# Kernel tuning notes

Measured on AMD Instinct MI355X. Metric: run time of the kernel, lower is better.

## Reference

```python
import jax, jax.numpy as jnp
import numpy as np

SR = 16000
BLOCK_SIZE = 160
N_WT = 64
WT_LEN = 512
SEC = 60
T = SR * SEC  # 960000 samples
FRAMES = 100 * SEC  # 6000 attention frames


def _make_sine_table(length, cycle, phase):
    i = np.arange(length, dtype=np.float32)
    wt = np.sin(cycle * 2 * np.pi * i / length + 2 * phase * np.pi).astype(np.float32)
    wt[-1] = wt[0]  # loop-closing trick: last sample = first sample
    return wt


def setup_inputs() -> dict:
    key = jax.random.key(0)
    k1, k2, k3, k4 = jax.random.split(key, 4)
    pitch = jax.random.uniform(k1, (1, T, 1), dtype=jnp.float32) * 360.0 + 40.0  # 40..400 Hz
    amplitude = jax.random.uniform(k2, (1, T, 1), dtype=jnp.float32)
    # wavetables: first 4 are fixed sine harmonics with wrapped endpoint, rest learned
    rng = np.random.default_rng(0)
    wts = np.asarray(jax.random.normal(k3, (N_WT, WT_LEN), dtype=jnp.float32)) * 0.01
    for idx in range(4):
        wts[idx] = _make_sine_table(WT_LEN, idx + 1, rng.uniform(0.0, 1.0))
    wts[4:, -1] = wts[4:, 0]  # wrap endpoint for learned tables too
    attention = jax.random.normal(k4, (N_WT, FRAMES), dtype=jnp.float32)
    return {
        "pitch": pitch,
        "amplitude": amplitude,
        "wavetables": jnp.asarray(wts),
        "attention": attention,
        "sec": SEC,
    }


def reference(pitch, amplitude, wavetables, attention, sec):
    L = wavetables.shape[1]
    freq = pitch.reshape(-1)  # [T], torch .squeeze()
    inc = freq / SR * L  # phase increment per sample
    # exclusive cumulative sum: cumsum(inc) - inc  (matches cumsum - increment[0] broadcast)
    idx = (jnp.cumsum(inc) - inc) % L  # [T]
    lo = jnp.floor(idx)
    hi = jnp.ceil(idx)
    alpha = idx - lo  # fractional part
    lo_i = lo.astype(jnp.int32)
    hi_i = hi.astype(jnp.int32) % L
    # tanh applied to learned tables (idx >= 4); fixed sine tables passed through
    wts_eff = jnp.concatenate([wavetables[:4], jnp.tanh(wavetables[4:])], axis=0)  # [64, L]
    w_lo = wts_eff[:, lo_i]  # [64, T] gather
    w_hi = wts_eff[:, hi_i]  # [64, T] gather
    osc = w_lo + alpha[None, :] * (w_hi - w_lo)  # [64, T] linear interp
    att = jax.nn.softmax(attention, axis=0)  # softmax over wavetables
    att_up = jnp.repeat(att, BLOCK_SIZE, axis=1)  # nearest-neighbor upsample -> [64, T]
    mixed = jnp.sum(osc * att_up, axis=0)  # [T]
    return mixed[None, :, None] * amplitude  # [1, T, 1]
```

## Files before the change

kernel.cpp:

```cpp
#include <hip/hip_runtime.h>
#include <math.h>

#define BLKSZ 160
#define NWT   64
#define WTLEN 512
#define FPB   8
#define SPB   1280
#define NTHR  256
#define SMP   12

#define NB1   3750
#define NB2   235
#define NB2P  240
#define NB3   15

#define PRI(a)  ((a) + ((a) >> 4))

static __device__ __forceinline__ float inc32_of(float p) {
    return (p / 16000.0f) * 512.0f;
}

__global__ __launch_bounds__(256) void k_leaf(
    const float* __restrict__ pitch, const float* __restrict__ wts,
    float* __restrict__ bs1, float* __restrict__ bs2,
    float* __restrict__ wts_eff, int T)
{
    int t = threadIdx.x;
    if (blockIdx.x >= NB2) {
        int i = (blockIdx.x - NB2) * 256 + t;
        if (i < NWT * WTLEN) {
            float v = wts[i];
            if ((i >> 9) >= 4) v = tanhf(v);
            wts_eff[i] = v;
        }
        return;
    }
    __shared__ float b0[256];
    __shared__ float b1[16];
    int blk = blockIdx.x;
    size_t s0 = (size_t)blk * 4096;
    int nsamp = min(4096, T - (int)s0);
    int nb0 = nsamp >> 4;
    if (t < nb0) {
        const float4* p4 = (const float4*)(pitch + s0 + (size_t)t * 16);
        float acc = 0.f;
        #pragma unroll
        for (int i = 0; i < 4; ++i) {
            float4 v = p4[i];
            acc = acc + inc32_of(v.x);
            acc = acc + inc32_of(v.y);
            acc = acc + inc32_of(v.z);
            acc = acc + inc32_of(v.w);
        }
        b0[t] = acc;
    }
    __syncthreads();
    int nb1 = nb0 >> 4;
    if (t < nb1) {
        float acc = b0[t * 16];
        for (int j = 1; j < 16; ++j) acc = acc + b0[t * 16 + j];
        b1[t] = acc;
        bs1[blk * 16 + t] = acc;
    }
    __syncthreads();
    if (t == 0) {
        float acc = b1[0];
        for (int j = 1; j < nb1; ++j) acc = acc + b1[j];
        bs2[blk] = acc;
    }
}

__global__ __launch_bounds__(256) void k_main(
    const float* __restrict__ pitch, const float* __restrict__ amp,
    const float* __restrict__ att, const float* __restrict__ wts_eff,
    const float* __restrict__ bs1g, const float* __restrict__ bs2g,
    float* __restrict__ out, int frames)
{
    __shared__ float smT[NWT][SMP];
    __shared__ float mixrow[FPB][WTLEN];
    __shared__ float pr[SPB + SPB / 16];
    __shared__ float roffL[SPB / 16];
    __shared__ float bs2L[NB2P];
    __shared__ float bs1w[32];
    __shared__ float bs3L[NB3];
    __shared__ float S4L[NB3];
    __shared__ float S3w[2];
    __shared__ float S2w[6];
    __shared__ float bs1prevL;

    int tid = threadIdx.x, lane = tid & 63, wv = tid >> 6;
    int b = blockIdx.x;
    int f0 = b * FPB;
    size_t base = (size_t)b * SPB;
    int j0 = 5 * b - 2;
    int rlo = max(j0, 0) >> 4;

    #pragma unroll
    for (int r = 0; r < 2; ++r) {
        int f = f0 + wv * 2 + r;
        float a = att[(size_t)lane * frames + f];
        float m = a;
        #pragma unroll
        for (int off = 32; off; off >>= 1) m = fmaxf(m, __shfl_xor(m, off, 64));
        float e = expf(a - m);
        float s = e;
        #pragma unroll
        for (int off = 32; off; off >>= 1) s += __shfl_xor(s, off, 64);
        smT[lane][wv * 2 + r] = e / s;
    }

    float increg[SPB / NTHR];
    #pragma unroll
    for (int i = 0; i < SPB / NTHR; ++i) {
        increg[i] = inc32_of(pitch[base + i * NTHR + tid]);
        pr[PRI(i * NTHR + tid)] = increg[i];
    }
    if (tid < NB2P) {
        bs2L[tid] = (tid < NB2) ? bs2g[tid] : 0.f;
    } else {
        int i = tid - NB2P;
        #pragma unroll
        for (int k = 0; k < 2; ++k) {
            int idx = i * 2 + k;
            int g = rlo * 16 + idx;
            bs1w[idx] = (g < NB1) ? bs1g[g] : 0.f;
        }
    }
    if (tid == 224) bs1prevL = (b > 0) ? bs1g[5 * b - 1] : 0.f;
    __syncthreads();

    if (tid < SPB / 16) {
        int a0 = tid * 17;
        float acc = pr[a0];
        for (int j = 1; j < 16; ++j) { acc = acc + pr[a0 + j]; pr[a0 + j] = acc; }
    } else if (tid >= 80 && tid < 80 + NB3) {
        int r = tid - 80;
        float a = bs2L[r * 16];
        for (int j = 1; j < 16; ++j) a = a + bs2L[r * 16 + j];
        bs3L[r] = a;
    }
    if (tid == 80) {
        float a = 0.f;
        for (int i = 0; i < NB3; ++i) { a = a + bs3L[i]; S4L[i] = a; }
    }
    if (tid >= 80 && tid < 82) {
        int r = rlo - 1 + (tid - 80);
        float v = 0.f;
        if (r >= 0 && r < NB2) {
            int g = r >> 4, p = r & 15;
            float a = bs2L[g * 16];
            for (int k = 1; k <= p; ++k) a = a + bs2L[g * 16 + k];
            v = g ? (a + S4L[g - 1]) : a;
        }
        S3w[tid - 80] = v;
    }
    if (tid >= 80 && tid < 86) {
        int j = j0 + (tid - 80);
        float v = 0.f;
        if (j >= 0) {
            int r = j >> 4, p = j & 15;
            int o = (r - rlo) * 16;
            float a = bs1w[o];
            for (int q = 1; q <= p; ++q) a = a + bs1w[o + q];
            v = r ? (a + S3w[r - rlo]) : a;
        }
        S2w[tid - 80] = v;
    }
    {
        #pragma unroll
        for (int it = 0; it < 2; ++it) {
            int j = tid + it * NTHR;
            float acc[FPB];
            #pragma unroll
            for (int k = 0; k < FPB; ++k) acc[k] = 0.f;
            for (int w = 0; w < NWT; ++w) {
                float v = wts_eff[w * WTLEN + j];
                float4 s0 = *(const float4*)&smT[w][0];
                float4 s1 = *(const float4*)&smT[w][4];
                acc[0] += s0.x * v;  acc[1] += s0.y * v;
                acc[2] += s0.z * v;  acc[3] += s0.w * v;
                acc[4] += s1.x * v;  acc[5] += s1.y * v;
                acc[6] += s1.z * v;  acc[7] += s1.w * v;
            }
            #pragma unroll
            for (int k = 0; k < FPB; ++k) mixrow[k][j] = acc[k];
        }
    }
    __syncthreads();

    if (tid < SPB / 16) {
        float v;
        if (tid == 0) {
            v = (b == 0) ? 0.f : (bs1prevL + S2w[0]);
        } else {
            int lr = (tid - 1) >> 4;
            int p  = (tid - 1) & 15;
            float acc = pr[(lr * 16) * 17 + 15];
            for (int q = 1; q <= p; ++q) acc = acc + pr[(lr * 16 + q) * 17 + 15];
            int gr = 5 * b + lr;
            v = gr ? (acc + S2w[lr + 1]) : acc;
        }
        roffL[tid] = v;
    }
    __syncthreads();

    #pragma unroll
    for (int i = 0; i < SPB / NTHR; ++i) {
        int tl = i * NTHR + tid;
        size_t tg = base + tl;
        float C = pr[PRI(tl)] + roffL[tl >> 4];
        float sub = C - increg[i];
        float idx = fmodf(sub, 512.0f);
        if (idx < 0.f) idx += 512.f;
        int li = (int)idx;
        float alpha = idx - (float)li;
        int hi = ((int)ceilf(idx)) & (WTLEN - 1);
        int fr = tl / BLKSZ;
        float wlo = mixrow[fr][li];
        float whi = mixrow[fr][hi];
        out[tg] = (wlo + alpha * (whi - wlo)) * amp[tg];
    }
}

extern "C" void kernel_launch(void* const* d_in, const int* in_sizes, int n_in,
                              void* d_out, int out_size, void* d_ws, size_t ws_size,
                              hipStream_t stream) {
    const float* pitch = (const float*)d_in[0];
    const float* amp   = (const float*)d_in[1];
    const float* wts   = (const float*)d_in[2];
    const float* att   = (const float*)d_in[3];

    int T      = in_sizes[0];
    int frames = T / BLKSZ;
    int nmain  = T / SPB;

    float* ws      = (float*)d_ws;
    float* wts_eff = ws;
    float* bs1     = ws + 32768;
    float* bs2     = ws + 32768 + 3840;
    float* out     = (float*)d_out;

    int nwts_blocks = (NWT * WTLEN + 255) / 256;
    k_leaf<<<NB2 + nwts_blocks, 256, 0, stream>>>(pitch, wts, bs1, bs2, wts_eff, T);
    k_main<<<nmain, 256, 0, stream>>>(pitch, amp, att, wts_eff, bs1, bs2, out, frames);
}
```

Before: 25.45 us.

## Compute per-sample prefix sums on the fly, removing a scan phase and barrier

The serial in-place row scan and the separate row-offset pass with its barrier are removed. Each sample thread now reads its 16-element row and the relevant block sums as float4 vectors and recomputes its own prefix with predicated adds. A padded row pitch of 20 keeps float4 loads aligned. This trades one __syncthreads and the serial phases for redundant arithmetic in every thread, while keeping the same sequential summation order.

```diff
diff --git a/kernel.cpp b/kernel.cpp
--- a/kernel.cpp
+++ b/kernel.cpp
@@ -8,13 +8,14 @@
 #define SPB   1280
 #define NTHR  256
 #define SMP   12
+#define RPITCH 20
 
 #define NB1   3750
 #define NB2   235
 #define NB2P  240
 #define NB3   15
 
-#define PRI(a)  ((a) + ((a) >> 4))
+#define PRI20(a)  ((((a) >> 4) * RPITCH) + ((a) & 15))
 
 static __device__ __forceinline__ float inc32_of(float p) {
     return (p / 16000.0f) * 512.0f;
@@ -70,6 +71,26 @@
     }
 }
 
+#define CHAIN16(acc, p, a0, a1, a2, a3)                         \
+    {                                                           \
+        acc = a0.x;                                             \
+        if ((p) >= 1)  acc = acc + a0.y;                        \
+        if ((p) >= 2)  acc = acc + a0.z;                        \
+        if ((p) >= 3)  acc = acc + a0.w;                        \
+        if ((p) >= 4)  acc = acc + a1.x;                        \
+        if ((p) >= 5)  acc = acc + a1.y;                        \
+        if ((p) >= 6)  acc = acc + a1.z;                        \
+        if ((p) >= 7)  acc = acc + a1.w;                        \
+        if ((p) >= 8)  acc = acc + a2.x;                        \
+        if ((p) >= 9)  acc = acc + a2.y;                        \
+        if ((p) >= 10) acc = acc + a2.z;                        \
+        if ((p) >= 11) acc = acc + a2.w;                        \
+        if ((p) >= 12) acc = acc + a3.x;                        \
+        if ((p) >= 13) acc = acc + a3.y;                        \
+        if ((p) >= 14) acc = acc + a3.z;                        \
+        if ((p) >= 15) acc = acc + a3.w;                        \
+    }
+
 __global__ __launch_bounds__(256) void k_main(
     const float* __restrict__ pitch, const float* __restrict__ amp,
     const float* __restrict__ att, const float* __restrict__ wts_eff,
@@ -78,8 +99,8 @@
 {
     __shared__ float smT[NWT][SMP];
     __shared__ float mixrow[FPB][WTLEN];
-    __shared__ float pr[SPB + SPB / 16];
-    __shared__ float roffL[SPB / 16];
+    __shared__ float pr[80 * RPITCH];
+    __shared__ float bs0L[80];
     __shared__ float bs2L[NB2P];
     __shared__ float bs1w[32];
     __shared__ float bs3L[NB3];
@@ -113,7 +134,7 @@
     #pragma unroll
     for (int i = 0; i < SPB / NTHR; ++i) {
         increg[i] = inc32_of(pitch[base + i * NTHR + tid]);
-        pr[PRI(i * NTHR + tid)] = increg[i];
+        pr[PRI20(i * NTHR + tid)] = increg[i];
     }
     if (tid < NB2P) {
         bs2L[tid] = (tid < NB2) ? bs2g[tid] : 0.f;
@@ -129,10 +150,12 @@
     if (tid == 224) bs1prevL = (b > 0) ? bs1g[5 * b - 1] : 0.f;
     __syncthreads();
 
-    if (tid < SPB / 16) {
-        int a0 = tid * 17;
-        float acc = pr[a0];
-        for (int j = 1; j < 16; ++j) { acc = acc + pr[a0 + j]; pr[a0 + j] = acc; }
+    if (tid < 80) {
+        const float4* r4 = (const float4*)&pr[tid * RPITCH];
+        float4 a0 = r4[0], a1 = r4[1], a2 = r4[2], a3 = r4[3];
+        float acc;
+        CHAIN16(acc, 15, a0, a1, a2, a3);
+        bs0L[tid] = acc;
     } else if (tid >= 80 && tid < 80 + NB3) {
         int r = tid - 80;
         float a = bs2L[r * 16];
@@ -188,27 +211,32 @@
     }
     __syncthreads();
 
-    if (tid < SPB / 16) {
-        float v;
-        if (tid == 0) {
-            v = (b == 0) ? 0.f : (bs1prevL + S2w[0]);
-        } else {
-            int lr = (tid - 1) >> 4;
-            int p  = (tid - 1) & 15;
-            float acc = pr[(lr * 16) * 17 + 15];
-            for (int q = 1; q <= p; ++q) acc = acc + pr[(lr * 16 + q) * 17 + 15];
-            int gr = 5 * b + lr;
-            v = gr ? (acc + S2w[lr + 1]) : acc;
-        }
-        roffL[tid] = v;
-    }
-    __syncthreads();
-
     #pragma unroll
     for (int i = 0; i < SPB / NTHR; ++i) {
         int tl = i * NTHR + tid;
         size_t tg = base + tl;
-        float C = pr[PRI(tl)] + roffL[tl >> 4];
+        int row = tl >> 4, p = tl & 15;
+
+        const float4* r4 = (const float4*)&pr[row * RPITCH];
+        float4 a0 = r4[0], a1 = r4[1], a2 = r4[2], a3 = r4[3];
+        float pref;
+        CHAIN16(pref, p, a0, a1, a2, a3);
+
+        float roffv;
+        if (row == 0) {
+            roffv = (b == 0) ? 0.f : (bs1prevL + S2w[0]);
+        } else {
+            int lr = (row - 1) >> 4;
+            int pp = (row - 1) & 15;
+            const float4* b4 = (const float4*)&bs0L[lr * 16];
+            float4 c0 = b4[0], c1 = b4[1], c2 = b4[2], c3 = b4[3];
+            float acc2;
+            CHAIN16(acc2, pp, c0, c1, c2, c3);
+            int gr = 5 * b + lr;
+            roffv = gr ? (acc2 + S2w[lr + 1]) : acc2;
+        }
+
+        float C = pref + roffv;
         float sub = C - increg[i];
         float idx = fmodf(sub, 512.0f);
         if (idx < 0.f) idx += 512.f;
```

Measured after the change: 27.72 us. 8.9% more time.
